# Performance work log

Hardware: AMD Instinct MI355X
Metric: run time of the kernel (lower is better)

## Reference

```python
import jax, jax.numpy as jnp
import numpy as np

N, C, H, W = 8, 256, 64, 64
EPS = 1e-5


def setup_inputs() -> dict:
    key = jax.random.key(0)
    ks = jax.random.split(key, 11)
    s = 0.02
    return {
        "x": jax.random.normal(ks[0], (N, C, H, W), dtype=jnp.float32),
        "ln_w": jnp.ones((C, H, W), dtype=jnp.float32),
        "ln_b": jnp.zeros((C, H, W), dtype=jnp.float32),
        "wq": jax.random.normal(ks[1], (C, C), dtype=jnp.float32) * s,
        "bq": jnp.zeros((C,), dtype=jnp.float32),
        "wk": jax.random.normal(ks[2], (C, C), dtype=jnp.float32) * s,
        "bk": jnp.zeros((C,), dtype=jnp.float32),
        "wv": jax.random.normal(ks[3], (C, C), dtype=jnp.float32) * s,
        "bv": jnp.zeros((C,), dtype=jnp.float32),
        "wo": jax.random.normal(ks[4], (C, C), dtype=jnp.float32) * s,
        "bo": jnp.zeros((C,), dtype=jnp.float32),
    }


def _conv1x1(x, w, b):
    # x: [n,c,h,w], w: [out,in], b: [out]  (1x1 conv == per-pixel matmul)
    return jnp.einsum("nchw,oc->nohw", x, w) + b[None, :, None, None]


def reference(x, ln_w, ln_b, wq, bq, wk, bk, wv, bv, wo, bo):
    n, c, h, w = x.shape
    # LayerNorm over (C,H,W)
    mu = jnp.mean(x, axis=(1, 2, 3), keepdims=True)
    var = jnp.var(x, axis=(1, 2, 3), keepdims=True)
    nx = (x - mu) * jax.lax.rsqrt(var + EPS) * ln_w[None] + ln_b[None]

    q = _conv1x1(nx, wq, bq).reshape(n, c, h * w)  # [n,c,hw]
    k = _conv1x1(nx, wk, bk).reshape(n, c, h * w)
    v = _conv1x1(nx, wv, bv).reshape(n, c, h * w)

    scale = 1.0 / jnp.sqrt(jnp.float32(c))
    qk = jnp.einsum("nci,ncj->nij", q, k) * scale       # [n,hw,hw]
    attn = jax.nn.softmax(qk, axis=-1)
    res = jnp.einsum("nij,ncj->nci", attn, v)           # [n,c,hw]
    res = res.reshape(n, c, h, w)
    res = _conv1x1(res, wo, bo)
    return x + res
```

## Files before the change

kernel.cpp:

```cpp
#include <hip/hip_runtime.h>
#include <hip/hip_bf16.h>

#define N_ 8
#define C_ 256
#define HW_ 4096
#define CNT_ (C_*HW_)

typedef __attribute__((ext_vector_type(8))) short bf16x8;
typedef __attribute__((ext_vector_type(4))) float f32x4;
typedef __attribute__((ext_vector_type(16))) float f32x16;
typedef __attribute__((ext_vector_type(4))) int i32x4;
typedef __attribute__((ext_vector_type(8))) int i32x8;

__device__ inline float exp2fast(float x){ return __builtin_amdgcn_exp2f(x); }

__device__ inline unsigned short f2bf(float f){
  union{float f; unsigned u;} v; v.f=f;
  unsigned r = v.u + 0x7fff + ((v.u>>16)&1);
  return (unsigned short)(r>>16);
}
__device__ inline float bf2f(unsigned short h){
  union{unsigned u; float f;} v; v.u = ((unsigned)h)<<16; return v.f;
}

__device__ inline f32x4 mfma16(bf16x8 a, bf16x8 b, f32x4 c){
  return __builtin_amdgcn_mfma_f32_16x16x32_bf16(a,b,c,0,0,0);
}
__device__ inline f32x16 mfma_mx(i32x8 a, i32x8 b, f32x16 c){
  return __builtin_amdgcn_mfma_scale_f32_32x32x64_f8f6f4(a, b, c, 0, 0, 0, 127, 0, 127);
}

__device__ inline i32x8 ld2x4(const char* p){
  i32x4 a = *(const i32x4*)p;
  i32x4 b = *(const i32x4*)(p+16);
  i32x8 r;
  r[0]=a[0]; r[1]=a[1]; r[2]=a[2]; r[3]=a[3];
  r[4]=b[0]; r[5]=b[1]; r[6]=b[2]; r[7]=b[3];
  return r;
}

#define GLL16(gp, lp) __builtin_amdgcn_global_load_lds( \
    (__attribute__((address_space(1))) void*)(gp), \
    (__attribute__((address_space(3))) void*)(lp), 16, 0, 0)

__global__ void k_cvtall(const float* __restrict__ s0, const float* __restrict__ s1,
                         const float* __restrict__ s2, const float* __restrict__ s3,
                         unsigned short* __restrict__ dst){
  int i = blockIdx.x*256 + threadIdx.x;
  const float* s = (i < 65536) ? s0 : (i < 131072) ? s1 : (i < 196608) ? s2 : s3;
  dst[i] = f2bf(s[i & 65535]);
}

__global__ void k_stats1(const float* __restrict__ x, float2* __restrict__ part){
  int n = blockIdx.x >> 8;
  int chunk = blockIdx.x & 255;
  const float4* p = (const float4*)(x + (size_t)n*CNT_ + (size_t)chunk*4096);
  int t = threadIdx.x;
  float s=0.f, s2=0.f;
  #pragma unroll
  for(int i=0;i<4;i++){
    float4 v = p[t + 256*i];
    s  += v.x+v.y+v.z+v.w;
    s2 += v.x*v.x+v.y*v.y+v.z*v.z+v.w*v.w;
  }
  #pragma unroll
  for(int o=32;o;o>>=1){ s += __shfl_down(s,o); s2 += __shfl_down(s2,o); }
  __shared__ float sh[4], sh2[4];
  int lane = t&63, wid = t>>6;
  if(lane==0){ sh[wid]=s; sh2[wid]=s2; }
  __syncthreads();
  if(t==0){
    float2 r; r.x = sh[0]+sh[1]+sh[2]+sh[3]; r.y = sh2[0]+sh2[1]+sh2[2]+sh2[3];
    part[blockIdx.x] = r;
  }
}

__global__ void k_norm(const float* __restrict__ x, const float* __restrict__ lnw,
                       const float* __restrict__ lnb, const float2* __restrict__ part,
                       unsigned short* __restrict__ nx){
  __shared__ float tile[64][65];
  __shared__ float2 stsh;
  int n = blockIdx.z, c0 = blockIdx.y*64, p0 = blockIdx.x*64;
  int t = threadIdx.x, col = t&63, rw = t>>6;
  {
    float2 v = part[n*256 + t];
    float s = v.x, s2 = v.y;
    #pragma unroll
    for(int o=32;o;o>>=1){ s += __shfl_down(s,o); s2 += __shfl_down(s2,o); }
    __shared__ float sh[4], sh2[4];
    int lane = t&63, wid = t>>6;
    if(lane==0){ sh[wid]=s; sh2[wid]=s2; }
    __syncthreads();
    if(t==0){
      s = sh[0]+sh[1]+sh[2]+sh[3];
      s2 = sh2[0]+sh2[1]+sh2[2]+sh2[3];
      float mean = s * (1.f/(float)CNT_);
      float var  = s2 * (1.f/(float)CNT_) - mean*mean;
      float2 r; r.x = mean; r.y = rsqrtf(var + 1e-5f);
      stsh = r;
    }
    __syncthreads();
  }
  float mu = stsh.x, rs = stsh.y;
  #pragma unroll
  for(int pass=0; pass<16; pass++){
    int row = pass*4 + rw;
    size_t gi = (size_t)(c0+row)*HW_ + (p0+col);
    float v = x[(size_t)n*CNT_ + gi];
    tile[row][col] = (v - mu)*rs*lnw[gi] + lnb[gi];
  }
  __syncthreads();
  #pragma unroll
  for(int pass=0; pass<16; pass++){
    int prow = pass*4 + rw;
    nx[((size_t)n*HW_ + p0+prow)*C_ + c0 + col] = f2bf(tile[col][prow]);
  }
}

__device__ inline void g2_stage(const char* A, const char* B, char* buf,
                                int w, int r8, int s8, int i0, int c0, int kb0){
  int sl = (s8 ^ (r8&7)) << 4;
  #pragma unroll
  for(int q=0;q<4;q++){
    int row = w*32 + q*8 + r8;
    GLL16(A + (size_t)(i0+row)*512 + kb0 + sl, buf + w*4096 + q*1024);
    GLL16(B + (size_t)(c0+row)*512 + kb0 + sl, buf + 16384 + w*4096 + q*1024);
  }
}

template<int BIAS_ROW, int OUT_MODE>
__global__ __launch_bounds__(256, 2) void k_gemm2(
    const unsigned short* __restrict__ Ab, long sA,
    const unsigned short* __restrict__ Bb, long sB,
    const float* __restrict__ bias, float scale,
    void* __restrict__ Outb, long sO, int ldo){
  __shared__ __align__(16) char lds[65536];
  int n = blockIdx.z;
  const char* A = (const char*)(Ab + (size_t)n*sA);
  const char* B = (const char*)(Bb + (size_t)n*sB);
  int t = threadIdx.x, w = t>>6, l = t&63;
  int wr = w>>1, wc = w&1, ri = l&15, kq = l>>4;
  int r8 = l>>3, s8 = l&7;
  int i0 = blockIdx.x*128, c0 = blockIdx.y*128;

  f32x4 acc[4][4];
  #pragma unroll
  for(int m=0;m<4;m++)
    #pragma unroll
    for(int nn=0;nn<4;nn++)
      #pragma unroll
      for(int r=0;r<4;r++) acc[m][nn][r] = 0.f;

  g2_stage(A, B, lds, w, r8, s8, i0, c0, 0);
  __syncthreads();

  for(int kt=0; kt<4; ++kt){
    char* buf = lds + (kt&1)*32768;
    if (kt < 3) g2_stage(A, B, lds + ((kt&1)^1)*32768, w, r8, s8, i0, c0, (kt+1)*128);
    __builtin_amdgcn_s_setprio(1);
    #pragma unroll
    for(int kc=0;kc<2;kc++){
      bf16x8 af[4], bfv[4];
      #pragma unroll
      for(int m=0;m<4;m++){
        int row = wr*64 + m*16 + ri;
        af[m] = *(const bf16x8*)(buf + row*128 + ((((kc<<2)|kq) ^ (row&7))<<4));
      }
      #pragma unroll
      for(int nn=0;nn<4;nn++){
        int row = wc*64 + nn*16 + ri;
        bfv[nn] = *(const bf16x8*)(buf + 16384 + row*128 + ((((kc<<2)|kq) ^ (row&7))<<4));
      }
      #pragma unroll
      for(int m=0;m<4;m++)
        #pragma unroll
        for(int nn=0;nn<4;nn++)
          acc[m][nn] = mfma16(af[m], bfv[nn], acc[m][nn]);
    }
    __builtin_amdgcn_s_setprio(0);
    __syncthreads();
  }

  if (OUT_MODE == 1){
    unsigned char* O8 = (unsigned char*)Outb + (size_t)n*sO;
    #pragma unroll
    for(int m=0;m<4;m++){
      #pragma unroll
      for(int nn=0;nn<4;nn++){
        #pragma unroll
        for(int r=0;r<4;r++){
          int row = i0 + wr*64 + m*16 + kq*4 + r;
          int col = c0 + wc*64 + nn*16 + ri;
          float d = (acc[m][nn][r] + bias[BIAS_ROW ? row : col])*scale;
          unsigned u;
          asm("v_cvt_pk_fp8_f32 %0, %1, %2" : "=v"(u) : "v"(d), "v"(0.f));
          O8[(size_t)row*ldo + col] = (unsigned char)(u & 0xff);
        }
      }
    }
  } else {
    unsigned short* O = (unsigned short*)Outb + (size_t)n*sO;
    #pragma unroll
    for(int m=0;m<4;m++){
      #pragma unroll
      for(int nn=0;nn<4;nn++){
        #pragma unroll
        for(int r=0;r<4;r++){
          int row = i0 + wr*64 + m*16 + kq*4 + r;
          int col = c0 + wc*64 + nn*16 + ri;
          float d = (acc[m][nn][r] + bias[BIAS_ROW ? row : col])*scale;
          O[(size_t)row*ldo + col] = f2bf(d);
        }
      }
    }
  }
}

__global__ __launch_bounds__(256, 2) void k_outproj2(
    const unsigned short* __restrict__ wob,
    const unsigned short* __restrict__ pO0, const unsigned short* __restrict__ pO1,
    const float2* __restrict__ pml,
    const float* __restrict__ bo, const float* __restrict__ x,
    float* __restrict__ out){
  __shared__ __align__(16) char lds[65536];
  int n = blockIdx.z;
  const char* A = (const char*)wob;
  const char* B0 = (const char*)(pO0 + (size_t)n*HW_*C_);
  const char* B1 = (const char*)(pO1 + (size_t)n*HW_*C_);
  int t = threadIdx.x, w = t>>6, l = t&63;
  int wr = w>>1, wc = w&1, ri = l&15, kq = l>>4;
  int r8 = l>>3, s8 = l&7;
  int i0 = blockIdx.x*128, c0 = blockIdx.y*128;
  int sl = (s8 ^ (r8&7)) << 4;

  float s0v[4], s1v[4];
  #pragma unroll
  for(int q=0;q<4;q++){
    int row = c0 + w*32 + q*8 + r8;
    float2 ml0 = pml[(size_t)n*HW_ + row];
    float2 ml1 = pml[(size_t)N_*HW_ + (size_t)n*HW_ + row];
    float mN = fmaxf(ml0.x, ml1.x);
    float a0 = exp2fast(ml0.x - mN), a1 = exp2fast(ml1.x - mN);
    float inv = 1.f/(a0*ml0.y + a1*ml1.y);
    s0v[q] = a0*inv; s1v[q] = a1*inv;
  }

  f32x4 acc[4][4];
  #pragma unroll
  for(int m=0;m<4;m++)
    #pragma unroll
    for(int nn=0;nn<4;nn++)
      #pragma unroll
      for(int r=0;r<4;r++) acc[m][nn][r] = 0.f;

  uint4 bl0[4], bl1[4];
  #pragma unroll
  for(int q=0;q<4;q++){
    int row = w*32 + q*8 + r8;
    GLL16(A + (size_t)(i0+row)*512 + sl, lds + w*4096 + q*1024);
    bl0[q] = *(const uint4*)(B0 + (size_t)(c0+row)*512 + sl);
    bl1[q] = *(const uint4*)(B1 + (size_t)(c0+row)*512 + sl);
  }
  #pragma unroll
  for(int q=0;q<4;q++){
    unsigned w0[4] = {bl0[q].x, bl0[q].y, bl0[q].z, bl0[q].w};
    unsigned w1[4] = {bl1[q].x, bl1[q].y, bl1[q].z, bl1[q].w};
    uint4 rw;
    unsigned rr[4];
    #pragma unroll
    for(int j=0;j<4;j++){
      float lo = s0v[q]*bf2f((unsigned short)(w0[j]&0xffff)) + s1v[q]*bf2f((unsigned short)(w1[j]&0xffff));
      float hi = s0v[q]*bf2f((unsigned short)(w0[j]>>16))    + s1v[q]*bf2f((unsigned short)(w1[j]>>16));
      rr[j] = (unsigned)f2bf(lo) | ((unsigned)f2bf(hi)<<16);
    }
    rw.x=rr[0]; rw.y=rr[1]; rw.z=rr[2]; rw.w=rr[3];
    *(uint4*)(lds + 16384 + w*4096 + q*1024 + l*16) = rw;
  }
  __syncthreads();

  for(int kt=0; kt<4; ++kt){
    char* buf  = lds + (kt&1)*32768;
    char* nbuf = lds + ((kt&1)^1)*32768;
    if (kt < 3){
      int kb0 = (kt+1)*128;
      #pragma unroll
      for(int q=0;q<4;q++){
        int row = w*32 + q*8 + r8;
        GLL16(A + (size_t)(i0+row)*512 + kb0 + sl, nbuf + w*4096 + q*1024);
        bl0[q] = *(const uint4*)(B0 + (size_t)(c0+row)*512 + kb0 + sl);
        bl1[q] = *(const uint4*)(B1 + (size_t)(c0+row)*512 + kb0 + sl);
      }
    }
    __builtin_amdgcn_s_setprio(1);
    #pragma unroll
    for(int kc=0;kc<2;kc++){
      bf16x8 af[4], bfv[4];
      #pragma unroll
      for(int m=0;m<4;m++){
        int row = wr*64 + m*16 + ri;
        af[m] = *(const bf16x8*)(buf + row*128 + ((((kc<<2)|kq) ^ (row&7))<<4));
      }
      #pragma unroll
      for(int nn=0;nn<4;nn++){
        int row = wc*64 + nn*16 + ri;
        bfv[nn] = *(const bf16x8*)(buf + 16384 + row*128 + ((((kc<<2)|kq) ^ (row&7))<<4));
      }
      #pragma unroll
      for(int m=0;m<4;m++)
        #pragma unroll
        for(int nn=0;nn<4;nn++)
          acc[m][nn] = mfma16(af[m], bfv[nn], acc[m][nn]);
    }
    __builtin_amdgcn_s_setprio(0);
    if (kt < 3){
      #pragma unroll
      for(int q=0;q<4;q++){
        unsigned w0[4] = {bl0[q].x, bl0[q].y, bl0[q].z, bl0[q].w};
        unsigned w1[4] = {bl1[q].x, bl1[q].y, bl1[q].z, bl1[q].w};
        unsigned rr[4];
        #pragma unroll
        for(int j=0;j<4;j++){
          float lo = s0v[q]*bf2f((unsigned short)(w0[j]&0xffff)) + s1v[q]*bf2f((unsigned short)(w1[j]&0xffff));
          float hi = s0v[q]*bf2f((unsigned short)(w0[j]>>16))    + s1v[q]*bf2f((unsigned short)(w1[j]>>16));
          rr[j] = (unsigned)f2bf(lo) | ((unsigned)f2bf(hi)<<16);
        }
        uint4 rw; rw.x=rr[0]; rw.y=rr[1]; rw.z=rr[2]; rw.w=rr[3];
        *(uint4*)(nbuf + 16384 + w*4096 + q*1024 + l*16) = rw;
      }
    }
    __syncthreads();
  }

  const float* xr = x + (size_t)n*CNT_;
  float* fout = out + (size_t)n*CNT_;
  #pragma unroll
  for(int m=0;m<4;m++){
    #pragma unroll
    for(int nn=0;nn<4;nn++){
      #pragma unroll
      for(int r=0;r<4;r++){
        int row = i0 + wr*64 + m*16 + kq*4 + r;
        int col = c0 + wc*64 + nn*16 + ri;
        size_t idx = (size_t)row*HW_ + col;
        fout[idx] = acc[m][nn][r] + bo[row] + xr[idx];
      }
    }
  }
}

__device__ inline void stage_KV_mx(const char* kb, const char* vb, char* buf,
                                   int w, int l, int j0){
  #pragma unroll
  for(int k=0;k<4;k++){
    int g = w*4 + k;
    int row = g*4 + (l>>4);
    int i = l & 15;
    int sp = (((i>>1) ^ (row&7))<<5) + ((i&1)<<4);
    GLL16(kb + (size_t)(j0+row)*256 + sp, buf + g*1024);
  }
  #pragma unroll
  for(int k=0;k<5;k++){
    int g = w*5 + k;
    int c = g*64 + l;
    int d = c/5; int sg = c - d*5; sg = (sg==4)?0:sg;
    GLL16(vb + (size_t)d*HW_ + j0 + sg*16, buf + 16384 + g*1024);
  }
}

__global__ __launch_bounds__(256, 2) void k_attn8(const unsigned char* __restrict__ qt,
                                                  const unsigned char* __restrict__ kt,
                                                  const unsigned char* __restrict__ vv,
                                                  unsigned short* __restrict__ pO0,
                                                  unsigned short* __restrict__ pO1,
                                                  float2* __restrict__ pml){
  __shared__ __align__(16) char lds[73728];
  int t = threadIdx.x, w = t>>6, l = t&63, hi = l>>5, lo5 = l&31;
  int nb = blockIdx.x & 7, rem = blockIdx.x >> 3;
  int qb = rem >> 1, jh = rem & 1;
  int q0 = qb*128 + w*32;
  const char* kb = (const char*)(kt + (size_t)nb*HW_*C_);
  const char* vb = (const char*)(vv + (size_t)nb*(size_t)CNT_);
  const char* qp = (const char*)(qt + (size_t)nb*HW_*C_);
  int jbase = jh*2048;

  i32x8 qfr[4];
  #pragma unroll
  for(int db=0; db<4; db++)
    qfr[db] = ld2x4(qp + (size_t)(q0+lo5)*256 + db*64 + hi*32);

  f32x16 o[8];
  #pragma unroll
  for(int dt=0;dt<8;dt++){
    #pragma unroll
    for(int r=0;r<16;r++) o[dt][r]=0.f;
  }
  float m = -1e30f, lsum = 0.f;

  stage_KV_mx(kb, vb, lds, w, l, jbase);
  __syncthreads();

  for(int it=0; it<32; ++it){
    char* bufc = lds + (it&1)*36864;
    if (it < 31) stage_KV_mx(kb, vb, lds + ((it&1)^1)*36864, w, l, jbase + (it+1)*64);

    f32x16 Sa, Sb;
    #pragma unroll
    for(int r=0;r<16;r++){ Sa[r]=0.f; Sb[r]=0.f; }
    __builtin_amdgcn_s_setprio(1);
    #pragma unroll
    for(int db=0; db<4; db++){
      int sl = ((db*2+hi) ^ (lo5&7))<<5;
      i32x8 ka  = ld2x4(bufc + lo5*256      + sl);
      i32x8 kb2 = ld2x4(bufc + (32+lo5)*256 + sl);
      Sa = mfma_mx(ka,  qfr[db], Sa);
      Sb = mfma_mx(kb2, qfr[db], Sb);
    }
    __builtin_amdgcn_s_setprio(0);

    float mm[8];
    #pragma unroll
    for(int r=0;r<8;r++) mm[r] = fmaxf(fmaxf(Sa[r],Sa[r+8]), fmaxf(Sb[r],Sb[r+8]));
    mm[0]=fmaxf(mm[0],mm[4]); mm[1]=fmaxf(mm[1],mm[5]);
    mm[2]=fmaxf(mm[2],mm[6]); mm[3]=fmaxf(mm[3],mm[7]);
    float mx = fmaxf(fmaxf(mm[0],mm[1]), fmaxf(mm[2],mm[3]));
    { float mA = mx, mB = mx;
      asm("v_permlane32_swap_b32 %0, %1" : "+v"(mA), "+v"(mB));
      mx = fmaxf(mA, mB); }
    if (!__all(mx <= m + 8.f)){
      float mn = fmaxf(m, mx);
      float al = exp2fast(m - mn);
      lsum *= al;
      #pragma unroll
      for(int dt=0;dt<8;dt++) o[dt] = o[dt] * al;
      m = mn;
    }
    float rs = 0.f;
    #pragma unroll
    for(int r=0;r<16;r++){
      Sa[r] = exp2fast(Sa[r]-m); rs += Sa[r];
      Sb[r] = exp2fast(Sb[r]-m); rs += Sb[r];
    }
    { float rA = rs, rB = rs;
      asm("v_permlane32_swap_b32 %0, %1" : "+v"(rA), "+v"(rB));
      lsum += rA + rB; }

    unsigned Aw[4], Bw[4];
    #pragma unroll
    for(int w4=0; w4<4; w4++){
      unsigned ua, ub;
      asm("v_cvt_pk_fp8_f32 %0, %1, %2" : "=v"(ua) : "v"(Sa[4*w4]), "v"(Sa[4*w4+1]));
      asm("v_cvt_pk_fp8_f32 %0, %1, %2 op_sel:[0,0,1]" : "+v"(ua) : "v"(Sa[4*w4+2]), "v"(Sa[4*w4+3]));
      asm("v_cvt_pk_fp8_f32 %0, %1, %2" : "=v"(ub) : "v"(Sb[4*w4]), "v"(Sb[4*w4+1]));
      asm("v_cvt_pk_fp8_f32 %0, %1, %2 op_sel:[0,0,1]" : "+v"(ub) : "v"(Sb[4*w4+2]), "v"(Sb[4*w4+3]));
      Aw[w4] = ua; Bw[w4] = ub;
    }
    #pragma unroll
    for(int w4=0; w4<4; w4++)
      asm("v_permlane32_swap_b32 %0, %1" : "+v"(Aw[w4]), "+v"(Bw[w4]));
    i32x8 P;
    P[0]=Aw[0]; P[1]=Bw[0]; P[2]=Aw[1]; P[3]=Bw[1];
    P[4]=Aw[2]; P[5]=Bw[2]; P[6]=Aw[3]; P[7]=Bw[3];

    __builtin_amdgcn_s_setprio(1);
    #pragma unroll
    for(int dt=0;dt<8;dt++){
      i32x8 vf = ld2x4(bufc + 16384 + (dt*32+lo5)*80 + hi*32);
      o[dt] = mfma_mx(vf, P, o[dt]);
    }
    __builtin_amdgcn_s_setprio(0);
    __syncthreads();
  }

  unsigned short* pb = (jh ? pO1 : pO0) + ((size_t)nb*HW_ + q0 + lo5)*C_;
  #pragma unroll
  for(int dt=0;dt<8;dt++){
    #pragma unroll
    for(int g=0;g<4;g++){
      int d0 = dt*32 + g*8 + hi*4;
      unsigned short h0 = f2bf(o[dt][4*g]);
      unsigned short h1 = f2bf(o[dt][4*g+1]);
      unsigned short h2 = f2bf(o[dt][4*g+2]);
      unsigned short h3 = f2bf(o[dt][4*g+3]);
      uint2 uo; uo.x = (unsigned)h0 | ((unsigned)h1<<16);
      uo.y = (unsigned)h2 | ((unsigned)h3<<16);
      *(uint2*)(pb + d0) = uo;
    }
  }
  if (l < 32){
    float2 ml; ml.x = m; ml.y = lsum;
    pml[(size_t)jh*((size_t)N_*HW_) + (size_t)nb*HW_ + q0 + lo5] = ml;
  }
}

extern "C" void kernel_launch(void* const* d_in, const int* in_sizes, int n_in,
                              void* d_out, int out_size, void* d_ws, size_t ws_size,
                              hipStream_t stream) {
  const float* x   = (const float*)d_in[0];
  const float* lnw = (const float*)d_in[1];
  const float* lnb = (const float*)d_in[2];
  const float* wq  = (const float*)d_in[3];
  const float* bq  = (const float*)d_in[4];
  const float* wk  = (const float*)d_in[5];
  const float* bk  = (const float*)d_in[6];
  const float* wv  = (const float*)d_in[7];
  const float* bv  = (const float*)d_in[8];
  const float* wo  = (const float*)d_in[9];
  const float* bo  = (const float*)d_in[10];
  float* out = (float*)d_out;

  uintptr_t base = (uintptr_t)d_ws;
  float2* part  = (float2*)base;
  unsigned short* wqb = (unsigned short*)(base + 16448);
  unsigned short* wkb = wqb + 65536;
  unsigned short* wvb = wqb + 2*65536;
  unsigned short* wob = wqb + 3*65536;
  unsigned short* nx  = wqb + 4*65536;
  const size_t TEN = (size_t)N_*HW_*C_;
  unsigned short* qtb = nx + TEN;
  unsigned short* ktb = qtb + TEN;
  unsigned short* vvb = ktb + TEN;
  unsigned short* pO1 = vvb + TEN;
  float2* pml = (float2*)(pO1 + TEN);
  unsigned short* pO0 = nx;

  k_cvtall<<<dim3(1024),256,0,stream>>>(wq, wk, wv, wo, wqb);

  k_stats1<<<dim3(2048),256,0,stream>>>(x, part);
  k_norm<<<dim3(64,4,8),256,0,stream>>>(x, lnw, lnb, part, nx);

  k_gemm2<0,1><<<dim3(32,2,8),256,0,stream>>>(nx, (long)(HW_*C_), wqb, 0L, bq, 0.3002807f,
                                              qtb, (long)(HW_*C_), C_);
  k_gemm2<0,1><<<dim3(32,2,8),256,0,stream>>>(nx, (long)(HW_*C_), wkb, 0L, bk, 0.3002807f,
                                              ktb, (long)(HW_*C_), C_);
  k_gemm2<1,1><<<dim3(2,32,8),256,0,stream>>>(wvb, 0L, nx, (long)(HW_*C_), bv, 1.0f,
                                              vvb, (long)(CNT_), HW_);

  k_attn8<<<dim3(512),256,0,stream>>>((const unsigned char*)qtb, (const unsigned char*)ktb,
                                      (const unsigned char*)vvb, pO0, pO1, pml);

  k_outproj2<<<dim3(2,32,8),256,0,stream>>>(wob, pO0, pO1, pml, bo, x, out);
}
```

Measured before the change: 163.8 us.

## Fuse Q/K projections into one GEMM and merge weight-convert with stats kernel

The separate weight-conversion and LayerNorm-statistics kernels are merged into one launch, which also packs the Q and K biases into a contiguous buffer. The Q and K projections become a single GEMM over the contiguous wq|wk weights, writing an interleaved [hw, 512] fp8 buffer. The attention kernel reads Q and K from that buffer with a 512-byte row stride. This removes two kernel launches and reads the normalized input once for both projections, at the cost of a wider-stride layout for the Q/K loads in attention.

```diff
diff --git a/kernel.cpp b/kernel.cpp
--- a/kernel.cpp
+++ b/kernel.cpp
@@ -43,19 +43,26 @@
     (__attribute__((address_space(1))) void*)(gp), \
     (__attribute__((address_space(3))) void*)(lp), 16, 0, 0)
 
-__global__ void k_cvtall(const float* __restrict__ s0, const float* __restrict__ s1,
-                         const float* __restrict__ s2, const float* __restrict__ s3,
-                         unsigned short* __restrict__ dst){
-  int i = blockIdx.x*256 + threadIdx.x;
-  const float* s = (i < 65536) ? s0 : (i < 131072) ? s1 : (i < 196608) ? s2 : s3;
-  dst[i] = f2bf(s[i & 65535]);
-}
-
-__global__ void k_stats1(const float* __restrict__ x, float2* __restrict__ part){
-  int n = blockIdx.x >> 8;
-  int chunk = blockIdx.x & 255;
+__global__ void k_pre(const float* __restrict__ wq, const float* __restrict__ wk,
+                      const float* __restrict__ wv, const float* __restrict__ wo,
+                      const float* __restrict__ bq, const float* __restrict__ bk,
+                      unsigned short* __restrict__ dst, float* __restrict__ bqk,
+                      const float* __restrict__ x, float2* __restrict__ part){
+  int bid = blockIdx.x, t = threadIdx.x;
+  if (bid < 1024){
+    int i = bid*256 + t;
+    const float* s = (i < 65536) ? wq : (i < 131072) ? wk : (i < 196608) ? wv : wo;
+    dst[i] = f2bf(s[i & 65535]);
+    return;
+  }
+  if (bid == 1024){
+    bqk[t] = bq[t];
+    bqk[256+t] = bk[t];
+    return;
+  }
+  int cid = bid - 1025;
+  int n = cid >> 8, chunk = cid & 255;
   const float4* p = (const float4*)(x + (size_t)n*CNT_ + (size_t)chunk*4096);
-  int t = threadIdx.x;
   float s=0.f, s2=0.f;
   #pragma unroll
   for(int i=0;i<4;i++){
@@ -71,7 +78,7 @@
   __syncthreads();
   if(t==0){
     float2 r; r.x = sh[0]+sh[1]+sh[2]+sh[3]; r.y = sh2[0]+sh2[1]+sh2[2]+sh2[3];
-    part[blockIdx.x] = r;
+    part[cid] = r;
   }
 }
 
@@ -265,7 +272,6 @@
   for(int q=0;q<4;q++){
     unsigned w0[4] = {bl0[q].x, bl0[q].y, bl0[q].z, bl0[q].w};
     unsigned w1[4] = {bl1[q].x, bl1[q].y, bl1[q].z, bl1[q].w};
-    uint4 rw;
     unsigned rr[4];
     #pragma unroll
     for(int j=0;j<4;j++){
@@ -273,7 +279,7 @@
       float hi = s0v[q]*bf2f((unsigned short)(w0[j]>>16))    + s1v[q]*bf2f((unsigned short)(w1[j]>>16));
       rr[j] = (unsigned)f2bf(lo) | ((unsigned)f2bf(hi)<<16);
     }
-    rw.x=rr[0]; rw.y=rr[1]; rw.z=rr[2]; rw.w=rr[3];
+    uint4 rw; rw.x=rr[0]; rw.y=rr[1]; rw.z=rr[2]; rw.w=rr[3];
     *(uint4*)(lds + 16384 + w*4096 + q*1024 + l*16) = rw;
   }
   __syncthreads();
@@ -356,7 +362,7 @@
     int row = g*4 + (l>>4);
     int i = l & 15;
     int sp = (((i>>1) ^ (row&7))<<5) + ((i&1)<<4);
-    GLL16(kb + (size_t)(j0+row)*256 + sp, buf + g*1024);
+    GLL16(kb + (size_t)(j0+row)*512 + sp, buf + g*1024);
   }
   #pragma unroll
   for(int k=0;k<5;k++){
@@ -367,8 +373,7 @@
   }
 }
 
-__global__ __launch_bounds__(256, 2) void k_attn8(const unsigned char* __restrict__ qt,
-                                                  const unsigned char* __restrict__ kt,
+__global__ __launch_bounds__(256, 2) void k_attn8(const unsigned char* __restrict__ qk8,
                                                   const unsigned char* __restrict__ vv,
                                                   unsigned short* __restrict__ pO0,
                                                   unsigned short* __restrict__ pO1,
@@ -378,15 +383,15 @@
   int nb = blockIdx.x & 7, rem = blockIdx.x >> 3;
   int qb = rem >> 1, jh = rem & 1;
   int q0 = qb*128 + w*32;
-  const char* kb = (const char*)(kt + (size_t)nb*HW_*C_);
+  const char* qp = (const char*)(qk8 + (size_t)nb*HW_*512);
+  const char* kb = qp + 256;
   const char* vb = (const char*)(vv + (size_t)nb*(size_t)CNT_);
-  const char* qp = (const char*)(qt + (size_t)nb*HW_*C_);
   int jbase = jh*2048;
 
   i32x8 qfr[4];
   #pragma unroll
   for(int db=0; db<4; db++)
-    qfr[db] = ld2x4(qp + (size_t)(q0+lo5)*256 + db*64 + hi*32);
+    qfr[db] = ld2x4(qp + (size_t)(q0+lo5)*512 + db*64 + hi*32);
 
   f32x16 o[8];
   #pragma unroll
@@ -510,32 +515,29 @@
 
   uintptr_t base = (uintptr_t)d_ws;
   float2* part  = (float2*)base;
-  unsigned short* wqb = (unsigned short*)(base + 16448);
+  float*  bqk   = (float*)(base + 16384);
+  unsigned short* wqb = (unsigned short*)(base + 18432);
   unsigned short* wkb = wqb + 65536;
   unsigned short* wvb = wqb + 2*65536;
   unsigned short* wob = wqb + 3*65536;
   unsigned short* nx  = wqb + 4*65536;
   const size_t TEN = (size_t)N_*HW_*C_;
-  unsigned short* qtb = nx + TEN;
-  unsigned short* ktb = qtb + TEN;
-  unsigned short* vvb = ktb + TEN;
+  unsigned short* qkb = nx + TEN;
+  unsigned short* vvb = qkb + TEN;
   unsigned short* pO1 = vvb + TEN;
   float2* pml = (float2*)(pO1 + TEN);
   unsigned short* pO0 = nx;
-
-  k_cvtall<<<dim3(1024),256,0,stream>>>(wq, wk, wv, wo, wqb);
-
-  k_stats1<<<dim3(2048),256,0,stream>>>(x, part);
+  (void)wkb;
+
+  k_pre<<<dim3(3073),256,0,stream>>>(wq, wk, wv, wo, bq, bk, wqb, bqk, x, part);
   k_norm<<<dim3(64,4,8),256,0,stream>>>(x, lnw, lnb, part, nx);
 
-  k_gemm2<0,1><<<dim3(32,2,8),256,0,stream>>>(nx, (long)(HW_*C_), wqb, 0L, bq, 0.3002807f,
-                                              qtb, (long)(HW_*C_), C_);
-  k_gemm2<0,1><<<dim3(32,2,8),256,0,stream>>>(nx, (long)(HW_*C_), wkb, 0L, bk, 0.3002807f,
-                                              ktb, (long)(HW_*C_), C_);
+  k_gemm2<0,1><<<dim3(32,4,8),256,0,stream>>>(nx, (long)(HW_*C_), wqb, 0L, bqk, 0.3002807f,
+                                              qkb, (long)(HW_*512), 512);
   k_gemm2<1,1><<<dim3(2,32,8),256,0,stream>>>(wvb, 0L, nx, (long)(HW_*C_), bv, 1.0f,
                                               vvb, (long)(CNT_), HW_);
 
-  k_attn8<<<dim3(512),256,0,stream>>>((const unsigned char*)qtb, (const unsigned char*)ktb,
+  k_attn8<<<dim3(512),256,0,stream>>>((const unsigned char*)qkb,
                                       (const unsigned char*)vvb, pO0, pO1, pml);
 
   k_outproj2<<<dim3(2,32,8),256,0,stream>>>(wob, pO0, pO1, pml, bo, x, out);
```

After: 150.9 us. 7.9% less time.
